# Kernel tuning notes

Measured on AMD Instinct MI355X. Metric: run time of the kernel, lower is better.

The kernel has to match this reference:

```python
import jax, jax.numpy as jnp
import numpy as np

B, D, WIN, SW = 256, 38, 640, 10
S = WIN // SW  # 64 time steps
EPS = 1e-5

def leaky(v):
    return jnp.where(v > 0, v, 0.01 * v)

def _ln(v, g, b):
    mu = v.mean(-1, keepdims=True)
    var = v.var(-1, keepdims=True)
    return g * (v - mu) / jnp.sqrt(var + EPS) + b

def setup_inputs():
    key = jax.random.key(0)
    ks = jax.random.split(key, 24)
    n = lambda k, shp, s=0.05: jax.random.normal(k, shp, jnp.float32) * s
    return {
        'x': jax.random.normal(ks[0], (B, D, WIN), jnp.float32),
        'W1': n(ks[1], (D, 64, SW)), 'b1': n(ks[2], (D, 64)),
        'W2': n(ks[3], (D, 4, 3)), 'b2': n(ks[4], (D, 4)),
        'Wl': n(ks[5], (D, 64, 124)), 'bl': n(ks[6], (D, 64)),
        'Wb1': n(ks[7], (64, 64)), 'bb1': n(ks[8], (64,)),
        'lng': jnp.ones((64,), jnp.float32), 'lnb': jnp.zeros((64,), jnp.float32),
        'Wb2': n(ks[9], (64, 64)), 'bb2': n(ks[10], (64,)),
        'Wq': n(ks[11], (1, 64)), 'bq': n(ks[12], (1,)),
        'Wk': n(ks[13], (D, 64)), 'bk': n(ks[14], (D,)),
        'Wv1': n(ks[15], (D, 32, 64)), 'bv1': n(ks[16], (D, 32)),
        'lnvg': jnp.ones((D, 32), jnp.float32), 'lnvb': jnp.zeros((D, 32), jnp.float32),
        'Wv2': n(ks[17], (D, 32)), 'bv2': n(ks[18], (D,)),
        'Wq2': n(ks[19], (1, 64 * D)), 'bq2': n(ks[20], (1,)),
        'Wk2': n(ks[21], (S, 64 * D)), 'bk2': n(ks[22], (S,)),
    }

def reference(x, W1, b1, W2, b2, Wl, bl, Wb1, bb1, lng, lnb, Wb2, bb2,
              Wq, bq, Wk, bk, Wv1, bv1, lnvg, lnvb, Wv2, bv2, Wq2, bq2, Wk2, bk2):
    Bsz = x.shape[0]
    # FE1: per-channel Conv1d(1,64,k=SW,stride=SW) == window-reshape + per-dim GEMM
    xw = x.reshape(Bsz, D, S, SW)
    f1 = leaky(jnp.einsum('bdsw,dow->bdso', xw, W1) + b1[None, :, None, :])  # [B,D,S,64]
    # FE2: per-channel Conv1d(1,4,k=3,p=1) over the 64 features
    xp = jnp.pad(f1, ((0, 0), (0, 0), (0, 0), (1, 1)))
    win = jnp.stack([xp[..., r:r + 64] for r in range(3)], -1)  # [B,D,S,64,3]
    c = leaky(jnp.einsum('bdstr,dcr->bdsct', win, W2) + b2[None, :, None, :, None])  # [B,D,S,4,64]
    # MaxPool1d(3, stride=2): 64 -> 31
    m = jnp.max(jnp.stack([c[..., s:s + 61:2] for s in range(3)], 0), 0)  # [B,D,S,4,31]
    e = leaky(jnp.einsum('bdsf,dof->bdso', m.reshape(Bsz, D, S, 124), Wl) + bl[None, :, None, :])  # embed [B,D,S,64]
    # BeforeInstanceEncoder (shared), recurrent accumulator == cumsum over time
    h = leaky(_ln(jnp.einsum('bdso,po->bdsp', e, Wb1) + bb1, lng, lnb))
    g = leaky(jnp.einsum('bdsp,qp->bdsq', h, Wb2) + bb2)
    acml = jnp.cumsum(g, axis=2)  # [B,D,S,64]
    wq = jax.nn.sigmoid(jnp.einsum('bdso,o->bds', e, Wq[0]) + bq[0])            # [B,D,S]
    wk = jax.nn.sigmoid(jnp.einsum('bdso,jo->bdsj', acml, Wk) + bk)             # [B,D,S,D]
    att1 = jax.nn.softmax(jnp.einsum('bks,bjsk->bsj', wq, wk) / np.float32(np.sqrt(D)), axis=-1)  # [B,S,D]
    v = leaky(_ln(jnp.einsum('bdso,dho->bdsh', e, Wv1) + bv1[None, :, None, :],
                  lnvg[None, :, None, :], lnvb[None, :, None, :]))
    wv = jax.nn.relu(jnp.einsum('bdsh,dh->bds', v, Wv2) + bv2[None, :, None])   # [B,D,S]
    cont1 = jnp.transpose(wv, (0, 2, 1)) * att1  # [B,S,D]
    contributes1 = cont1[..., None]              # [B,S,D,1]
    output1 = cont1.sum(-1, keepdims=True)       # [B,S,1]
    # bag-level attention over time
    ef = jnp.transpose(e, (0, 2, 1, 3)).reshape(Bsz, S, D * 64)
    wq_a = jax.nn.sigmoid(ef @ Wq2.T + bq2)[..., 0]  # [B,S]
    wk_a = jax.nn.sigmoid(ef @ Wk2.T + bk2)          # [B,S,S]
    att2 = jax.nn.softmax(jnp.einsum('bs,bts->bt', wq_a, wk_a) / np.float32(np.sqrt(WIN)), axis=-1)  # [B,S]
    contributes2 = output1 * att2[..., None]  # [B,S,1]
    output2 = contributes2.sum(1)             # [B,1]
    return (output2, contributes2, contributes1)
```

## Files before the change

### kernel.cpp

```cpp
#include <hip/hip_runtime.h>
#include <math.h>

#define Bv 256
#define Dv 38
#define Sv 64
#define SWv 10
#define EPSv 1e-5f

typedef float f4 __attribute__((ext_vector_type(4)));

__device__ __forceinline__ float leaky(float v){ return v > 0.f ? v : 0.01f*v; }
__device__ __forceinline__ float sigm(float v){ return 1.f/(1.f+expf(-v)); }

__device__ __forceinline__ float wred64(float v){
  #pragma unroll
  for (int off=32; off; off>>=1) v += __shfl_xor(v, off, 64);
  return v;
}
__device__ __forceinline__ float wmax64(float v){
  #pragma unroll
  for (int off=32; off; off>>=1) v = fmaxf(v, __shfl_xor(v, off, 64));
  return v;
}

__global__ __launch_bounds__(256) void k0_pack(
    const float* __restrict__ Wl, const float* __restrict__ W1,
    const float* __restrict__ Wv1,
    float* __restrict__ wlT, float* __restrict__ w1T, float* __restrict__ wv1T)
{
  int idx = blockIdx.x*256 + threadIdx.x;
  if (idx < 330752) {
    int d = idx / 8704, r = idx % 8704;
    int c = r / 1088, rr = r % 1088;
    int q = rr / 68, o = rr % 68;
    int ch = q >> 2, io = q & 3, fi = 4*c + io;
    float v = 0.f;
    if (o < 64 && fi <= 30) v = Wl[d*7936 + o*124 + ch*31 + fi];
    wlT[idx] = v;
  } else if (idx < 330752 + 25840) {
    int t = idx - 330752;
    int d = t / 680, rr = t % 680;
    int w = rr / 68, o = rr % 68;
    w1T[t] = (o < 64) ? W1[d*640 + o*10 + w] : 0.f;
  } else if (idx < 330752 + 25840 + 87552) {
    int t = idx - 330752 - 25840;
    int d = t / 2304, rr = t % 2304;
    int o = rr / 36, h = rr % 36;
    wv1T[t] = (h < 32) ? Wv1[d*2048 + h*64 + o] : 0.f;
  }
}

__global__ __launch_bounds__(256, 3) void k1_fe4(
    const float* __restrict__ x,
    const float* __restrict__ w1T_all, const float* __restrict__ b1,
    const float* __restrict__ W2, const float* __restrict__ b2,
    const float* __restrict__ wlT_all, const float* __restrict__ bl,
    const float* __restrict__ Wq, const float* __restrict__ bq,
    const float* __restrict__ wv1T_all, const float* __restrict__ bv1,
    const float* __restrict__ lnvg, const float* __restrict__ lnvb,
    const float* __restrict__ Wv2, const float* __restrict__ bv2,
    const float* __restrict__ Wq2,
    float* __restrict__ e_ws, float* __restrict__ wq2_ws, float* __restrict__ wv_ws,
    float* __restrict__ wqa_p)
{
  __shared__ float sm[12688];
  const int d  = blockIdx.x >> 7;
  const int b0 = (blockIdx.x & 127) * 2;
  const int tid = threadIdx.x;
  const int z = tid >> 7;
  const int t = tid & 127;
  const int tx = t & 15, ty = t >> 4;
  const int wz = ty >> 2;
  const int bd = (b0 + z)*Dv + d;
  const float bq0 = bq[0];

#define PJ(j) ((j) < 4 ? 4*ty + (j) : 32 + 4*ty + ((j)-4))

  if (tid < 64) {
    sm[12032+tid] = b1[d*64+tid];
    sm[12096+tid] = bl[d*64+tid];
    sm[12160+tid] = Wq[tid];
    sm[12368+tid] = Wq2[d*64+tid];
  } else if (tid < 96) {
    int u = tid-64;
    sm[12240+u]=bv1[d*32+u]; sm[12272+u]=lnvg[d*32+u];
    sm[12304+u]=lnvb[d*32+u]; sm[12336+u]=Wv2[d*32+u];
  } else if (tid < 108) sm[12224+(tid-96)] = W2[d*12+(tid-96)];
  else if (tid < 112)   sm[12236+(tid-108)] = b2[d*4+(tid-108)];

  {
    const f4* s4 = (const f4*)(w1T_all + (size_t)d*680);
    if (tid < 170) ((f4*)&sm[9792])[tid] = s4[tid];
  }
  for (int i = tid; i < 1280; i += 256) {
    int z2 = i / 640, tt = i % 640;
    sm[10472 + z2*680 + (tt%10)*68 + tt/10] =
      x[((size_t)((b0+z2)*Dv + d))*640 + tt];
  }
  const f4* wlsrc = (const f4*)(wlT_all + (size_t)d*8704);
  {
    ((f4*)&sm[8704])[tid] = wlsrc[tid];
    if (tid < 16) ((f4*)&sm[8704])[tid+256] = wlsrc[tid+256];
  }
  __syncthreads();

  float fe[4][8];
  #pragma unroll
  for (int i=0;i<4;++i)
    #pragma unroll
    for (int j=0;j<8;++j) fe[i][j]=0.f;
  #pragma unroll
  for (int w = 0; w < 10; ++w) {
    f4 a   = *(const f4*)&sm[10472 + z*680 + w*68 + 4*tx];
    f4 blo = *(const f4*)&sm[9792 + w*68 + 4*ty];
    f4 bhi = *(const f4*)&sm[9792 + w*68 + 32 + 4*ty];
    #pragma unroll
    for (int i=0;i<4;++i)
      #pragma unroll
      for (int j=0;j<8;++j) fe[i][j] += a[i]*((j<4)?blo[j&3]:bhi[j&3]);
  }
  #pragma unroll
  for (int j=0;j<8;++j) {
    int o = PJ(j);
    float bb = sm[12032+o];
    f4 v = {leaky(fe[0][j]+bb), leaky(fe[1][j]+bb), leaky(fe[2][j]+bb), leaky(fe[3][j]+bb)};
    *(f4*)&sm[z*4352 + o*68 + 4*tx] = v;
  }
  __syncthreads();

  float ea[4][8];
  #pragma unroll
  for (int i=0;i<4;++i)
    #pragma unroll
    for (int j=0;j<8;++j) ea[i][j]=0.f;

  f4 wr0, wr1;
  for (int c = 0; c < 8; ++c) {
    if (c > 0) {
      ((f4*)&sm[8704])[tid] = wr0;
      if (tid < 16) ((f4*)&sm[8704])[tid+256] = wr1;
    }
    {
      int sg = t & 15, io = (t >> 4) & 3, chh = t >> 6;
      int fi = 4*c + io;
      if (fi <= 30) {
        int t0 = 2*fi - 1;
        const float* fsrc = &sm[z*4352];
        f4 v0;
        if (fi == 0) { v0[0]=0.f; v0[1]=0.f; v0[2]=0.f; v0[3]=0.f; }
        else         { v0 = *(const f4*)&fsrc[t0*68 + 4*sg]; }
        f4 v1 = *(const f4*)&fsrc[(t0+1)*68 + 4*sg];
        f4 v2 = *(const f4*)&fsrc[(t0+2)*68 + 4*sg];
        f4 v3 = *(const f4*)&fsrc[(t0+3)*68 + 4*sg];
        f4 v4 = *(const f4*)&fsrc[(t0+4)*68 + 4*sg];
        float* mdst = &sm[9792 + z*1088];
        #pragma unroll
        for (int cc2 = 0; cc2 < 2; ++cc2) {
          int ch = 2*chh + cc2;
          float w0=sm[12224+ch*3], w1=sm[12224+ch*3+1], w2=sm[12224+ch*3+2];
          float bb=sm[12236+ch];
          f4 r;
          #pragma unroll
          for (int e2=0;e2<4;++e2) {
            float ca = bb + v0[e2]*w0 + v1[e2]*w1 + v2[e2]*w2;
            float cb = bb + v1[e2]*w0 + v2[e2]*w1 + v3[e2]*w2;
            float cc = bb + v2[e2]*w0 + v3[e2]*w1 + v4[e2]*w2;
            r[e2] = fmaxf(fmaxf(leaky(ca),leaky(cb)),leaky(cc));
          }
          *(f4*)&mdst[(ch*4+io)*68 + 4*sg] = r;
        }
      }
    }
    if (c < 7) {
      wr0 = wlsrc[(c+1)*272 + tid];
      if (tid < 16) wr1 = wlsrc[(c+1)*272 + 256 + tid];
    }
    __syncthreads();
    {
      const float* ma = &sm[9792 + z*1088];
      #pragma unroll
      for (int q=0;q<16;++q){
        f4 a   = *(const f4*)&ma[q*68+4*tx];
        f4 blo = *(const f4*)&sm[8704 + q*68+4*ty];
        f4 bhi = *(const f4*)&sm[8704 + q*68+32+4*ty];
        #pragma unroll
        for (int i=0;i<4;++i)
          #pragma unroll
          for (int j=0;j<8;++j) ea[i][j] += a[i]*((j<4)?blo[j&3]:bhi[j&3]);
      }
    }
    __syncthreads();
  }

  float ev[4][8];
  #pragma unroll
  for (int i=0;i<4;++i)
    #pragma unroll
    for (int j=0;j<8;++j) ev[i][j] = leaky(ea[i][j] + sm[12096 + PJ(j)]);

  {
    float* erow = e_ws + (size_t)bd * 4096;
    #pragma unroll
    for (int i=0;i<4;++i) {
      f4 lo = {ev[i][0],ev[i][1],ev[i][2],ev[i][3]};
      f4 hi = {ev[i][4],ev[i][5],ev[i][6],ev[i][7]};
      *(f4*)&erow[(4*tx+i)*64 + 4*ty] = lo;
      *(f4*)&erow[(4*tx+i)*64 + 32 + 4*ty] = hi;
    }
  }
  #pragma unroll
  for (int j=0;j<8;++j) {
    int o = PJ(j);
    f4 v = {ev[0][j],ev[1][j],ev[2][j],ev[3][j]};
    *(f4*)&sm[z*4352 + o*68 + 4*tx] = v;
  }
  #pragma unroll
  for (int i=0;i<4;++i) {
    float p = 0.f, pa = 0.f;
    #pragma unroll
    for (int j=0;j<8;++j) {
      p  += ev[i][j]*sm[12160 + PJ(j)];
      pa += ev[i][j]*sm[12368 + PJ(j)];
    }
    p += __shfl_xor(p, 16);  p += __shfl_xor(p, 32);
    pa += __shfl_xor(pa, 16); pa += __shfl_xor(pa, 32);
    if ((ty & 3) == 0) {
      sm[11520 + z*128 + wz*64 + 4*tx + i] = p;
      sm[12432 + z*128 + wz*64 + 4*tx + i] = pa;
    }
  }
  {
    const f4* s4 = (const f4*)(wv1T_all + (size_t)d*2304);
    f4 a0 = s4[tid], a1 = s4[tid+256];
    ((f4*)&sm[8704])[tid] = a0;
    ((f4*)&sm[8704])[tid+256] = a1;
    if (tid < 64) ((f4*)&sm[8704])[tid+512] = s4[tid+512];
  }
  __syncthreads();

  if (tid < 128) {
    int z2 = tid >> 6, r = tid & 63;
    float p = sm[11520 + z2*128 + r] + sm[11520 + z2*128 + 64 + r];
    wq2_ws[((size_t)(b0+z2)*64 + r)*Dv + d] = sigm(p + bq0);
    float pa = sm[12432 + z2*128 + r] + sm[12432 + z2*128 + 64 + r];
    wqa_p[((size_t)(b0+z2)*64 + r)*Dv + d] = pa;
  }

  float va[4][4];
  #pragma unroll
  for (int i=0;i<4;++i)
    #pragma unroll
    for (int j=0;j<4;++j) va[i][j]=0.f;
  #pragma unroll 8
  for (int o = 0; o < 64; ++o) {
    f4 a  = *(const f4*)&sm[z*4352 + o*68 + 4*tx];
    f4 bb = *(const f4*)&sm[8704 + o*36 + 4*ty];
    #pragma unroll
    for (int i=0;i<4;++i)
      #pragma unroll
      for (int j=0;j<4;++j) va[i][j] += a[i]*bb[j];
  }
  #pragma unroll
  for (int i=0;i<4;++i)
    #pragma unroll
    for (int j=0;j<4;++j) va[i][j] += sm[12240 + 4*ty + j];

  #pragma unroll
  for (int i=0;i<4;++i) {
    float ps=0.f, pq=0.f;
    #pragma unroll
    for (int j=0;j<4;++j) { ps += va[i][j]; pq += va[i][j]*va[i][j]; }
    ps += __shfl_xor(ps, 16); ps += __shfl_xor(ps, 32);
    pq += __shfl_xor(pq, 16); pq += __shfl_xor(pq, 32);
    if ((ty & 3) == 0) {
      sm[11008 + z*128 + wz*64 + 4*tx + i] = ps;
      sm[11264 + z*128 + wz*64 + 4*tx + i] = pq;
    }
  }
  __syncthreads();
  if (tid < 128) {
    int z2 = tid >> 6, r = tid & 63;
    float s_ = sm[11008 + z2*128 + r] + sm[11008 + z2*128 + 64 + r];
    float q_ = sm[11264 + z2*128 + r] + sm[11264 + z2*128 + 64 + r];
    float mu = s_*(1.f/32.f);
    float vr = q_*(1.f/32.f) - mu*mu;
    sm[11776 + z2*64 + r] = mu;
    sm[11904 + z2*64 + r] = rsqrtf(vr + EPSv);
  }
  __syncthreads();

  #pragma unroll
  for (int i=0;i<4;++i) {
    float mu = sm[11776 + z*64 + 4*tx + i];
    float rs = sm[11904 + z*64 + 4*tx + i];
    float p = 0.f;
    #pragma unroll
    for (int j=0;j<4;++j) {
      int h = 4*ty + j;
      float vh = leaky(sm[12272+h]*(va[i][j]-mu)*rs + sm[12304+h]);
      p += vh*sm[12336+h];
    }
    p += __shfl_xor(p, 16);
    p += __shfl_xor(p, 32);
    if ((ty & 3) == 0) sm[11520 + z*128 + wz*64 + 4*tx + i] = p;
  }
  __syncthreads();
  if (tid < 128) {
    int z2 = tid >> 6, r = tid & 63;
    float p = sm[11520 + z2*128 + r] + sm[11520 + z2*128 + 64 + r];
    wv_ws[((size_t)((b0+z2)*Dv + d))*64 + r] = fmaxf(p + bv2[d], 0.f);
  }
#undef PJ
}

__global__ __launch_bounds__(256) void k2_fused(
    const float* __restrict__ e_ws,
    const float* __restrict__ Wb1, const float* __restrict__ bb1,
    const float* __restrict__ lng, const float* __restrict__ lnb,
    const float* __restrict__ Wb2, const float* __restrict__ bb2,
    const float* __restrict__ Wk, const float* __restrict__ bk,
    const float* __restrict__ wq2_ws, float* __restrict__ score1)
{
  __shared__ float smem[14080];
  float* bufA = smem;
  float* bufB = smem + 8448;
  float* pts  = smem + 12544;
  float* ptq  = smem + 13184;
  float* stmu = smem + 13824;
  float* strs = smem + 13952;

  const int tid = threadIdx.x;
  const int tx = tid & 31;
  const int ty = tid >> 5;
  const int wid = tid >> 6;
  const int lane = tid & 63;
  const int bd0 = blockIdx.x * 2;
  const int bd1 = bd0 + 1;

#define PJ(j) ((j) < 4 ? 4*ty + (j) : 32 + 4*ty + ((j)-4))

  const int r0 = tid & 15, c0 = tid >> 4;

  f4 w2r[4];
  {
    const f4* W2src = (const f4*)Wb2;
    #pragma unroll
    for (int q = 0; q < 4; ++q) w2r[q] = W2src[(r0+16*q)*16 + c0];
  }

  {
    const f4* Esrc  = (const f4*)(e_ws + (size_t)bd0 * 4096);
    #pragma unroll
    for (int q = 0; q < 8; ++q) {
      int r = r0 + 16*q;
      f4 v = Esrc[r*16 + c0];
      #pragma unroll
      for (int k = 0; k < 4; ++k) bufA[(4*c0+k)*132 + r] = v[k];
    }
    const f4* W1src = (const f4*)Wb1;
    #pragma unroll
    for (int q = 0; q < 4; ++q) {
      int rr = r0 + 16*q;
      f4 v1 = W1src[rr*16 + c0];
      #pragma unroll
      for (int k = 0; k < 4; ++k) bufB[(4*c0+k)*64 + rr] = v1[k];
    }
  }
  __syncthreads();

  float bb1v[8], lngv[8], lnbv[8], bb2v[8];
  #pragma unroll
  for (int j=0;j<8;++j) {
    int p = PJ(j);
    bb1v[j]=bb1[p]; lngv[j]=lng[p]; lnbv[j]=lnb[p]; bb2v[j]=bb2[p];
  }

  float h[4][8];
  #pragma unroll
  for (int i=0;i<4;++i)
    #pragma unroll
    for (int j=0;j<8;++j) h[i][j]=0.f;
  for (int o = 0; o < 64; ++o) {
    f4 a  = *(const f4*)(bufA + o*132 + 4*tx);
    f4 bl = *(const f4*)(bufB + o*64 + 4*ty);
    f4 bh = *(const f4*)(bufB + o*64 + 32 + 4*ty);
    #pragma unroll
    for (int i=0;i<4;++i)
      #pragma unroll
      for (int j=0;j<8;++j) h[i][j] += a[i]*((j<4)?bl[j&3]:bh[j&3]);
  }
  #pragma unroll
  for (int i=0;i<4;++i)
    #pragma unroll
    for (int j=0;j<8;++j) h[i][j] += bb1v[j];

  #pragma unroll
  for (int i=0;i<4;++i) {
    float ps=0.f, pq=0.f;
    #pragma unroll
    for (int j=0;j<8;++j) { ps += h[i][j]; pq += h[i][j]*h[i][j]; }
    ps += __shfl_xor(ps, 32);
    pq += __shfl_xor(pq, 32);
    if (lane < 32) { pts[(4*tx+i)*5 + wid] = ps; ptq[(4*tx+i)*5 + wid] = pq; }
  }
  __syncthreads();

  {
    #pragma unroll
    for (int q = 0; q < 4; ++q) {
      int rr = r0 + 16*q;
      f4 v = w2r[q];
      #pragma unroll
      for (int k = 0; k < 4; ++k) bufB[(4*c0+k)*64 + rr] = v[k];
    }
  }
  float wkr[10];
  #pragma unroll
  for (int n = 0; n < 10; ++n) {
    int i2 = tid + 256*n;
    int q = i2/40, k = i2%40;
    wkr[n] = (k < Dv) ? Wk[k*64 + q] : 0.f;
  }
  if (tid < 128) {
    float s = pts[tid*5]+pts[tid*5+1]+pts[tid*5+2]+pts[tid*5+3];
    float q = ptq[tid*5]+ptq[tid*5+1]+ptq[tid*5+2]+ptq[tid*5+3];
    float mu = s*(1.f/64.f);
    float va = q*(1.f/64.f) - mu*mu;
    stmu[tid] = mu;
    strs[tid] = rsqrtf(va + EPSv);
  }
  __syncthreads();

  {
    float muv[4], rsv[4];
    #pragma unroll
    for (int i=0;i<4;++i) { muv[i]=stmu[4*tx+i]; rsv[i]=strs[4*tx+i]; }
    #pragma unroll
    for (int j=0;j<8;++j) {
      f4 v;
      #pragma unroll
      for (int i=0;i<4;++i)
        v[i] = leaky(lngv[j]*(h[i][j]-muv[i])*rsv[i] + lnbv[j]);
      *(f4*)&bufA[PJ(j)*132 + 4*tx] = v;
    }
  }
  __syncthreads();

  float g[4][8];
  #pragma unroll
  for (int i=0;i<4;++i)
    #pragma unroll
    for (int j=0;j<8;++j) g[i][j]=0.f;
  for (int p = 0; p < 64; ++p) {
    f4 a  = *(const f4*)(bufA + p*132 + 4*tx);
    f4 bl = *(const f4*)(bufB + p*64 + 4*ty);
    f4 bh = *(const f4*)(bufB + p*64 + 32 + 4*ty);
    #pragma unroll
    for (int i=0;i<4;++i)
      #pragma unroll
      for (int j=0;j<8;++j) g[i][j] += a[i]*((j<4)?bl[j&3]:bh[j&3]);
  }
  #pragma unroll
  for (int i=0;i<4;++i)
    #pragma unroll
    for (int j=0;j<8;++j) g[i][j] = leaky(g[i][j] + bb2v[j]);

  #pragma unroll
  for (int j=0;j<8;++j) {
    float c0_=g[0][j], c1=c0_+g[1][j], c2=c1+g[2][j], c3=c2+g[3][j];
    float incl = c3;
    #pragma unroll
    for (int dd=1; dd<16; dd<<=1) {
      float t = __shfl_up(incl, dd, 16);
      if ((tid & 15) >= dd) incl += t;
    }
    float ex = incl - c3;
    g[0][j]=ex+c0_; g[1][j]=ex+c1; g[2][j]=ex+c2; g[3][j]=ex+c3;
  }
  __syncthreads();

  #pragma unroll
  for (int j=0;j<8;++j) {
    f4 v = {g[0][j], g[1][j], g[2][j], g[3][j]};
    *(f4*)&bufA[PJ(j)*132 + 4*tx] = v;
  }
  #pragma unroll
  for (int n = 0; n < 10; ++n) bufB[tid + 256*n] = wkr[n];
  __syncthreads();

  float u[4][4], u2[4][4];
  #pragma unroll
  for (int i=0;i<4;++i)
    #pragma unroll
    for (int j=0;j<4;++j) { u[i][j]=0.f; u2[i][j]=0.f; }
  for (int q = 0; q < 64; ++q) {
    f4 a   = *(const f4*)(bufA + q*132 + 4*tx);
    f4 b1v = *(const f4*)(bufB + q*40 + 4*ty);
    #pragma unroll
    for (int i=0;i<4;++i)
      #pragma unroll
      for (int j=0;j<4;++j) u[i][j] += a[i]*b1v[j];
    if (ty < 2) {
      f4 b2v = *(const f4*)(bufB + q*40 + 32 + 4*ty);
      #pragma unroll
      for (int i=0;i<4;++i)
        #pragma unroll
        for (int j=0;j<4;++j) u2[i][j] += a[i]*b2v[j];
    }
  }

  const int b0g = bd0/Dv, d0g = bd0%Dv, b1g = bd1/Dv, d1g = bd1%Dv;
  #pragma unroll
  for (int i=0;i<4;++i) {
    int r = 4*tx + i;
    int s = r & 63;
    int bb_ = (r >> 6) ? b1g : b0g;
    const float* wqrow = wq2_ws + ((size_t)bb_*Sv + s)*Dv;
    float p = 0.f;
    #pragma unroll
    for (int j=0;j<4;++j) {
      int k = 4*ty + j;
      p += sigm(u[i][j] + bk[k]) * wqrow[k];
    }
    if (ty < 2) {
      #pragma unroll
      for (int j=0;j<4;++j) {
        int k = 32 + 4*ty + j;
        if (k < Dv) p += sigm(u2[i][j] + bk[k]) * wqrow[k];
      }
    }
    p += __shfl_xor(p, 32);
    if (lane < 32) pts[r*5 + wid] = p;
  }
  __syncthreads();
  if (tid < 128) {
    float tot = pts[tid*5]+pts[tid*5+1]+pts[tid*5+2]+pts[tid*5+3];
    int grp = tid >> 6, s = tid & 63;
    int bb_ = grp ? b1g : b0g;
    int dd_ = grp ? d1g : d0g;
    score1[((size_t)bb_*Sv + s)*Dv + dd_] = tot;
  }
#undef PJ
}

__global__ __launch_bounds__(64) void k3_att1(
    const float* __restrict__ score1, const float* __restrict__ wv_ws,
    const float* __restrict__ wqa_p, const float* __restrict__ bq2,
    float* __restrict__ out_c1, float* __restrict__ output1, float* __restrict__ wq_a)
{
  const int blk = blockIdx.x;
  const int b = blk / Sv, s = blk % Sv;
  const int lane = threadIdx.x;

  const float invsq = 0.16222142113076254f;
  float sc = (lane<Dv) ? score1[(b*Sv+s)*Dv+lane]*invsq : -1e30f;
  float mx = wmax64(sc);
  float ex = (lane<Dv) ? expf(sc-mx) : 0.f;
  float den = wred64(ex);
  float att = ex/den;
  float c1 = 0.f;
  if (lane<Dv) {
    c1 = wv_ws[(b*Dv+lane)*Sv+s]*att;
    out_c1[(b*Sv+s)*Dv+lane] = c1;
  }
  float tot = wred64(c1);
  if (lane==0) output1[b*Sv+s] = tot;

  float p = (lane < Dv) ? wqa_p[((size_t)b*Sv + s)*Dv + lane] : 0.f;
  p = wred64(p);
  if (lane==0) wq_a[b*Sv+s] = sigm(p + bq2[0]);
}

__global__ __launch_bounds__(256) void k4_gemm(
    const float* __restrict__ e_ws, const float* __restrict__ Wk2, const float* __restrict__ bk2,
    const float* __restrict__ wq_a, float* __restrict__ score2)
{
  const int b = blockIdx.x;
  const int tid = threadIdx.x;
  const int tx = tid & 15, ty = tid >> 4;
  __shared__ float AsT[64*68];
  __shared__ float BsT[64*68];
  __shared__ float pt[64*17];

  float acc[4][4];
  #pragma unroll
  for (int i=0;i<4;++i)
    #pragma unroll
    for (int j=0;j<4;++j) acc[i][j]=0.f;

  const int r0 = tid & 15, oc0 = tid >> 4;
  const f4* Bsrc = (const f4*)Wk2;

  for (int d = 0; d < 38; ++d) {
    const f4* Asrc = (const f4*)(e_ws + ((size_t)(b*Dv+d))*4096);
    #pragma unroll
    for (int q = 0; q < 4; ++q) {
      int r = r0 + 16*q;
      f4 av = Asrc[r*16 + oc0];
      f4 bv = Bsrc[(size_t)r*608 + d*16 + oc0];
      #pragma unroll
      for (int k = 0; k < 4; ++k) {
        AsT[(4*oc0+k)*68 + r] = av[k];
        BsT[(4*oc0+k)*68 + r] = bv[k];
      }
    }
    __syncthreads();
    #pragma unroll 4
    for (int o = 0; o < 64; ++o) {
      f4 a  = *(const f4*)&AsT[o*68 + 4*tx];
      f4 bb = *(const f4*)&BsT[o*68 + 4*ty];
      #pragma unroll
      for (int i=0;i<4;++i)
        #pragma unroll
        for (int j=0;j<4;++j) acc[i][j] += a[i]*bb[j];
    }
    __syncthreads();
  }

  #pragma unroll
  for (int i=0;i<4;++i) {
    float p = 0.f;
    #pragma unroll
    for (int j=0;j<4;++j) {
      int s = 4*ty + j;
      p += sigm(acc[i][j] + bk2[s]) * wq_a[b*Sv + s];
    }
    pt[(4*tx+i)*17 + ty] = p;
  }
  __syncthreads();
  if (tid < 64) {
    float tot = 0.f;
    #pragma unroll
    for (int y=0;y<16;++y) tot += pt[tid*17+y];
    score2[b*Sv + tid] = tot;
  }
}

__global__ __launch_bounds__(64) void k5_final(
    const float* __restrict__ score2, const float* __restrict__ output1,
    float* __restrict__ out)
{
  const int b = blockIdx.x;
  const int lane = threadIdx.x;
  const float inv = 0.039528470752104741f;
  float v = score2[b*Sv+lane]*inv;
  float mx = wmax64(v);
  float ex = expf(v-mx);
  float den = wred64(ex);
  float att = ex/den;
  float c2 = output1[b*Sv+lane]*att;
  out[256 + b*Sv + lane] = c2;
  float tot = wred64(c2);
  if (lane==0) out[b] = tot;
}

extern "C" void kernel_launch(void* const* d_in, const int* in_sizes, int n_in,
                              void* d_out, int out_size, void* d_ws, size_t ws_size,
                              hipStream_t stream)
{
  const float* x    = (const float*)d_in[0];
  const float* W1   = (const float*)d_in[1];
  const float* b1   = (const float*)d_in[2];
  const float* W2   = (const float*)d_in[3];
  const float* b2   = (const float*)d_in[4];
  const float* Wl   = (const float*)d_in[5];
  const float* bl   = (const float*)d_in[6];
  const float* Wb1  = (const float*)d_in[7];
  const float* bb1  = (const float*)d_in[8];
  const float* lng  = (const float*)d_in[9];
  const float* lnb  = (const float*)d_in[10];
  const float* Wb2  = (const float*)d_in[11];
  const float* bb2  = (const float*)d_in[12];
  const float* Wq   = (const float*)d_in[13];
  const float* bq   = (const float*)d_in[14];
  const float* Wk   = (const float*)d_in[15];
  const float* bk   = (const float*)d_in[16];
  const float* Wv1  = (const float*)d_in[17];
  const float* bv1  = (const float*)d_in[18];
  const float* lnvg = (const float*)d_in[19];
  const float* lnvb = (const float*)d_in[20];
  const float* Wv2  = (const float*)d_in[21];
  const float* bv2  = (const float*)d_in[22];
  const float* Wq2  = (const float*)d_in[23];
  const float* bq2  = (const float*)d_in[24];
  const float* Wk2  = (const float*)d_in[25];
  const float* bk2  = (const float*)d_in[26];

  float* ws = (float*)d_ws;
  float* e_ws  = ws;
  float* wq2w  = e_ws + (size_t)Bv*Dv*Sv*64;
  float* wv_ws = wq2w + (size_t)Bv*Sv*Dv;
  float* sc1   = wv_ws + (size_t)Bv*Dv*Sv;
  float* out1  = sc1 + (size_t)Bv*Sv*Dv;
  float* wqa   = out1 + (size_t)Bv*Sv;
  float* sc2   = wqa + (size_t)Bv*Sv;
  float* wlT   = sc2 + (size_t)Bv*Sv;
  float* w1T   = wlT + 330752;
  float* wv1T  = w1T + 25840;
  float* wqap  = wv1T + 87552;

  float* out = (float*)d_out;
  float* out_c1 = out + 256 + Bv*Sv;

  hipLaunchKernelGGL(k0_pack, dim3(1736), dim3(256), 0, stream,
    Wl, W1, Wv1, wlT, w1T, wv1T);
  hipLaunchKernelGGL(k1_fe4, dim3(Dv*128), dim3(256), 0, stream,
    x, w1T, b1, W2, b2, wlT, bl, Wq, bq, wv1T, bv1, lnvg, lnvb, Wv2, bv2,
    Wq2, e_ws, wq2w, wv_ws, wqap);
  hipLaunchKernelGGL(k2_fused, dim3(Bv*Dv/2), dim3(256), 0, stream,
    e_ws, Wb1, bb1, lng, lnb, Wb2, bb2, Wk, bk, wq2w, sc1);
  hipLaunchKernelGGL(k3_att1, dim3(Bv*Sv), dim3(64), 0, stream,
    sc1, wv_ws, wqap, bq2, out_c1, out1, wqa);
  hipLaunchKernelGGL(k4_gemm, dim3(Bv), dim3(256), 0, stream,
    e_ws, Wk2, bk2, wqa, sc2);
  hipLaunchKernelGGL(k5_final, dim3(Bv), dim3(64), 0, stream, sc2, out1, out);
}
```

Baseline: 663.5 us.

## Store embeddings transposed and pre-pack weights to remove in-kernel transposes

The embedding workspace is now written feature-major by the feature-extraction kernel, and Wb1, Wb2, Wk and Wk2 are pre-transposed in the packing kernel. Downstream kernels can then stage tiles into shared memory with contiguous vector stores instead of scalar transposing scatters. LayerNorm partial sums are now accumulated with shared-memory atomics rather than per-wave slots plus a reduction pass, which removes one barrier. The cost is a larger packing kernel, about 150K extra packed floats in the workspace, and shared atomics in k2.

```diff
diff --git a/kernel.cpp b/kernel.cpp
--- a/kernel.cpp
+++ b/kernel.cpp
@@ -25,8 +25,12 @@
 
 __global__ __launch_bounds__(256) void k0_pack(
     const float* __restrict__ Wl, const float* __restrict__ W1,
-    const float* __restrict__ Wv1,
-    float* __restrict__ wlT, float* __restrict__ w1T, float* __restrict__ wv1T)
+    const float* __restrict__ Wv1, const float* __restrict__ Wb1,
+    const float* __restrict__ Wb2, const float* __restrict__ Wk,
+    const float* __restrict__ Wk2,
+    float* __restrict__ wlT, float* __restrict__ w1T, float* __restrict__ wv1T,
+    float* __restrict__ wb1T, float* __restrict__ wb2T, float* __restrict__ wkT,
+    float* __restrict__ wk2T)
 {
   int idx = blockIdx.x*256 + threadIdx.x;
   if (idx < 330752) {
@@ -37,16 +41,33 @@
     float v = 0.f;
     if (o < 64 && fi <= 30) v = Wl[d*7936 + o*124 + ch*31 + fi];
     wlT[idx] = v;
-  } else if (idx < 330752 + 25840) {
+  } else if (idx < 356592) {
     int t = idx - 330752;
     int d = t / 680, rr = t % 680;
     int w = rr / 68, o = rr % 68;
     w1T[t] = (o < 64) ? W1[d*640 + o*10 + w] : 0.f;
-  } else if (idx < 330752 + 25840 + 87552) {
-    int t = idx - 330752 - 25840;
+  } else if (idx < 444144) {
+    int t = idx - 356592;
     int d = t / 2304, rr = t % 2304;
     int o = rr / 36, h = rr % 36;
     wv1T[t] = (h < 32) ? Wv1[d*2048 + h*64 + o] : 0.f;
+  } else if (idx < 448240) {
+    int t = idx - 444144;
+    int o = t >> 6, p = t & 63;
+    wb1T[t] = Wb1[p*64 + o];
+  } else if (idx < 452336) {
+    int t = idx - 448240;
+    int p = t >> 6, q = t & 63;
+    wb2T[t] = Wb2[q*64 + p];
+  } else if (idx < 454896) {
+    int t = idx - 452336;
+    int q = t / 40, k = t % 40;
+    wkT[t] = (k < Dv) ? Wk[k*64 + q] : 0.f;
+  } else if (idx < 610544) {
+    int t = idx - 454896;
+    int d = t / 4096, rr = t % 4096;
+    int o = rr >> 6, s = rr & 63;
+    wk2T[t] = Wk2[s*2432 + d*64 + o];
   }
 }
 
@@ -60,7 +81,7 @@
     const float* __restrict__ lnvg, const float* __restrict__ lnvb,
     const float* __restrict__ Wv2, const float* __restrict__ bv2,
     const float* __restrict__ Wq2,
-    float* __restrict__ e_ws, float* __restrict__ wq2_ws, float* __restrict__ wv_ws,
+    float* __restrict__ e_wsT, float* __restrict__ wq2_ws, float* __restrict__ wv_ws,
     float* __restrict__ wqa_p)
 {
   __shared__ float sm[12688];
@@ -199,13 +220,11 @@
     for (int j=0;j<8;++j) ev[i][j] = leaky(ea[i][j] + sm[12096 + PJ(j)]);
 
   {
-    float* erow = e_ws + (size_t)bd * 4096;
-    #pragma unroll
-    for (int i=0;i<4;++i) {
-      f4 lo = {ev[i][0],ev[i][1],ev[i][2],ev[i][3]};
-      f4 hi = {ev[i][4],ev[i][5],ev[i][6],ev[i][7]};
-      *(f4*)&erow[(4*tx+i)*64 + 4*ty] = lo;
-      *(f4*)&erow[(4*tx+i)*64 + 32 + 4*ty] = hi;
+    float* erow = e_wsT + (size_t)bd * 4096;
+    #pragma unroll
+    for (int j=0;j<8;++j) {
+      f4 v = {ev[0][j],ev[1][j],ev[2][j],ev[3][j]};
+      *(f4*)&erow[PJ(j)*64 + 4*tx] = v;
     }
   }
   #pragma unroll
@@ -314,56 +333,51 @@
 }
 
 __global__ __launch_bounds__(256) void k2_fused(
-    const float* __restrict__ e_ws,
-    const float* __restrict__ Wb1, const float* __restrict__ bb1,
+    const float* __restrict__ e_wsT,
+    const float* __restrict__ wb1T, const float* __restrict__ bb1,
     const float* __restrict__ lng, const float* __restrict__ lnb,
-    const float* __restrict__ Wb2, const float* __restrict__ bb2,
-    const float* __restrict__ Wk, const float* __restrict__ bk,
+    const float* __restrict__ wb2T, const float* __restrict__ bb2,
+    const float* __restrict__ wkT, const float* __restrict__ bk,
     const float* __restrict__ wq2_ws, float* __restrict__ score1)
 {
-  __shared__ float smem[14080];
+  __shared__ float smem[12864];
   float* bufA = smem;
   float* bufB = smem + 8448;
   float* pts  = smem + 12544;
-  float* ptq  = smem + 13184;
-  float* stmu = smem + 13824;
-  float* strs = smem + 13952;
+  float* ptq  = smem + 12704;
 
   const int tid = threadIdx.x;
   const int tx = tid & 31;
   const int ty = tid >> 5;
-  const int wid = tid >> 6;
   const int lane = tid & 63;
   const int bd0 = blockIdx.x * 2;
   const int bd1 = bd0 + 1;
 
 #define PJ(j) ((j) < 4 ? 4*ty + (j) : 32 + 4*ty + ((j)-4))
 
-  const int r0 = tid & 15, c0 = tid >> 4;
+  if (tid < 128) { pts[tid] = 0.f; ptq[tid] = 0.f; }
 
   f4 w2r[4];
   {
-    const f4* W2src = (const f4*)Wb2;
-    #pragma unroll
-    for (int q = 0; q < 4; ++q) w2r[q] = W2src[(r0+16*q)*16 + c0];
+    const f4* s4 = (const f4*)wb2T;
+    #pragma unroll
+    for (int q = 0; q < 4; ++q) w2r[q] = s4[tid + 256*q];
   }
 
   {
-    const f4* Esrc  = (const f4*)(e_ws + (size_t)bd0 * 4096);
-    #pragma unroll
-    for (int q = 0; q < 8; ++q) {
-      int r = r0 + 16*q;
-      f4 v = Esrc[r*16 + c0];
-      #pragma unroll
-      for (int k = 0; k < 4; ++k) bufA[(4*c0+k)*132 + r] = v[k];
-    }
-    const f4* W1src = (const f4*)Wb1;
-    #pragma unroll
-    for (int q = 0; q < 4; ++q) {
-      int rr = r0 + 16*q;
-      f4 v1 = W1src[rr*16 + c0];
-      #pragma unroll
-      for (int k = 0; k < 4; ++k) bufB[(4*c0+k)*64 + rr] = v1[k];
+    const f4* Esrc = (const f4*)(e_wsT + (size_t)bd0 * 4096);
+    #pragma unroll
+    for (int m = 0; m < 8; ++m) {
+      int n = tid + 256*m;
+      int o = n >> 5, t5 = n & 31;
+      int z = t5 >> 4, sg = t5 & 15;
+      *(f4*)&bufA[o*132 + z*64 + 4*sg] = Esrc[z*1024 + o*16 + sg];
+    }
+    const f4* W1s = (const f4*)wb1T;
+    #pragma unroll
+    for (int m = 0; m < 4; ++m) {
+      int n = tid + 256*m;
+      ((f4*)bufB)[n] = W1s[n];
     }
   }
   __syncthreads();
@@ -401,40 +415,26 @@
     for (int j=0;j<8;++j) { ps += h[i][j]; pq += h[i][j]*h[i][j]; }
     ps += __shfl_xor(ps, 32);
     pq += __shfl_xor(pq, 32);
-    if (lane < 32) { pts[(4*tx+i)*5 + wid] = ps; ptq[(4*tx+i)*5 + wid] = pq; }
+    if (lane < 32) {
+      atomicAdd(&pts[4*tx+i], ps);
+      atomicAdd(&ptq[4*tx+i], pq);
+    }
   }
   __syncthreads();
 
   {
     #pragma unroll
-    for (int q = 0; q < 4; ++q) {
-      int rr = r0 + 16*q;
-      f4 v = w2r[q];
-      #pragma unroll
-      for (int k = 0; k < 4; ++k) bufB[(4*c0+k)*64 + rr] = v[k];
-    }
-  }
-  float wkr[10];
-  #pragma unroll
-  for (int n = 0; n < 10; ++n) {
-    int i2 = tid + 256*n;
-    int q = i2/40, k = i2%40;
-    wkr[n] = (k < Dv) ? Wk[k*64 + q] : 0.f;
-  }
-  if (tid < 128) {
-    float s = pts[tid*5]+pts[tid*5+1]+pts[tid*5+2]+pts[tid*5+3];
-    float q = ptq[tid*5]+ptq[tid*5+1]+ptq[tid*5+2]+ptq[tid*5+3];
-    float mu = s*(1.f/64.f);
-    float va = q*(1.f/64.f) - mu*mu;
-    stmu[tid] = mu;
-    strs[tid] = rsqrtf(va + EPSv);
-  }
-  __syncthreads();
-
+    for (int q = 0; q < 4; ++q) ((f4*)bufB)[tid + 256*q] = w2r[q];
+  }
   {
     float muv[4], rsv[4];
     #pragma unroll
-    for (int i=0;i<4;++i) { muv[i]=stmu[4*tx+i]; rsv[i]=strs[4*tx+i]; }
+    for (int i=0;i<4;++i) {
+      float s = pts[4*tx+i], q = ptq[4*tx+i];
+      float mu = s*(1.f/64.f);
+      float va = q*(1.f/64.f) - mu*mu;
+      muv[i] = mu; rsv[i] = rsqrtf(va + EPSv);
+    }
     #pragma unroll
     for (int j=0;j<8;++j) {
       f4 v;
@@ -445,6 +445,8 @@
     }
   }
   __syncthreads();
+
+  if (tid < 128) pts[tid] = 0.f;
 
   float g[4][8];
   #pragma unroll
@@ -477,6 +479,10 @@
     float ex = incl - c3;
     g[0][j]=ex+c0_; g[1][j]=ex+c1; g[2][j]=ex+c2; g[3][j]=ex+c3;
   }
+
+  float wkr[10];
+  #pragma unroll
+  for (int n = 0; n < 10; ++n) wkr[n] = wkT[tid + 256*n];
   __syncthreads();
 
   #pragma unroll
@@ -530,11 +536,11 @@
       }
     }
     p += __shfl_xor(p, 32);
-    if (lane < 32) pts[r*5 + wid] = p;
+    if (lane < 32) atomicAdd(&pts[r], p);
   }
   __syncthreads();
   if (tid < 128) {
-    float tot = pts[tid*5]+pts[tid*5+1]+pts[tid*5+2]+pts[tid*5+3];
+    float tot = pts[tid];
     int grp = tid >> 6, s = tid & 63;
     int bb_ = grp ? b1g : b0g;
     int dd_ = grp ? d1g : d0g;
@@ -572,7 +578,8 @@
 }
 
 __global__ __launch_bounds__(256) void k4_gemm(
-    const float* __restrict__ e_ws, const float* __restrict__ Wk2, const float* __restrict__ bk2,
+    const float* __restrict__ e_wsT, const float* __restrict__ wk2T,
+    const float* __restrict__ bk2,
     const float* __restrict__ wq_a, float* __restrict__ score2)
 {
   const int b = blockIdx.x;
@@ -588,21 +595,15 @@
     #pragma unroll
     for (int j=0;j<4;++j) acc[i][j]=0.f;
 
-  const int r0 = tid & 15, oc0 = tid >> 4;
-  const f4* Bsrc = (const f4*)Wk2;
-
   for (int d = 0; d < 38; ++d) {
-    const f4* Asrc = (const f4*)(e_ws + ((size_t)(b*Dv+d))*4096);
-    #pragma unroll
-    for (int q = 0; q < 4; ++q) {
-      int r = r0 + 16*q;
-      f4 av = Asrc[r*16 + oc0];
-      f4 bv = Bsrc[(size_t)r*608 + d*16 + oc0];
-      #pragma unroll
-      for (int k = 0; k < 4; ++k) {
-        AsT[(4*oc0+k)*68 + r] = av[k];
-        BsT[(4*oc0+k)*68 + r] = bv[k];
-      }
+    const f4* Asrc = (const f4*)(e_wsT + ((size_t)(b*Dv+d))*4096);
+    const f4* Bsrc = (const f4*)(wk2T + (size_t)d*4096);
+    #pragma unroll
+    for (int m = 0; m < 4; ++m) {
+      int n = tid + 256*m;
+      int o = n >> 4, sg = n & 15;
+      *(f4*)&AsT[o*68 + 4*sg] = Asrc[n];
+      *(f4*)&BsT[o*68 + 4*sg] = Bsrc[n];
     }
     __syncthreads();
     #pragma unroll 4
@@ -687,8 +688,8 @@
   const float* bk2  = (const float*)d_in[26];
 
   float* ws = (float*)d_ws;
-  float* e_ws  = ws;
-  float* wq2w  = e_ws + (size_t)Bv*Dv*Sv*64;
+  float* e_wsT = ws;
+  float* wq2w  = e_wsT + (size_t)Bv*Dv*Sv*64;
   float* wv_ws = wq2w + (size_t)Bv*Sv*Dv;
   float* sc1   = wv_ws + (size_t)Bv*Dv*Sv;
   float* out1  = sc1 + (size_t)Bv*Sv*Dv;
@@ -698,20 +699,24 @@
   float* w1T   = wlT + 330752;
   float* wv1T  = w1T + 25840;
   float* wqap  = wv1T + 87552;
+  float* wb1T  = wqap + (size_t)Bv*Sv*Dv;
+  float* wb2T  = wb1T + 4096;
+  float* wkT   = wb2T + 4096;
+  float* wk2T  = wkT + 2560;
 
   float* out = (float*)d_out;
   float* out_c1 = out + 256 + Bv*Sv;
 
-  hipLaunchKernelGGL(k0_pack, dim3(1736), dim3(256), 0, stream,
-    Wl, W1, Wv1, wlT, w1T, wv1T);
+  hipLaunchKernelGGL(k0_pack, dim3(2385), dim3(256), 0, stream,
+    Wl, W1, Wv1, Wb1, Wb2, Wk, Wk2, wlT, w1T, wv1T, wb1T, wb2T, wkT, wk2T);
   hipLaunchKernelGGL(k1_fe4, dim3(Dv*128), dim3(256), 0, stream,
     x, w1T, b1, W2, b2, wlT, bl, Wq, bq, wv1T, bv1, lnvg, lnvb, Wv2, bv2,
-    Wq2, e_ws, wq2w, wv_ws, wqap);
+    Wq2, e_wsT, wq2w, wv_ws, wqap);
   hipLaunchKernelGGL(k2_fused, dim3(Bv*Dv/2), dim3(256), 0, stream,
-    e_ws, Wb1, bb1, lng, lnb, Wb2, bb2, Wk, bk, wq2w, sc1);
+    e_wsT, wb1T, bb1, lng, lnb, wb2T, bb2, wkT, bk, wq2w, sc1);
   hipLaunchKernelGGL(k3_att1, dim3(Bv*Sv), dim3(64), 0, stream,
     sc1, wv_ws, wqap, bq2, out_c1, out1, wqa);
   hipLaunchKernelGGL(k4_gemm, dim3(Bv), dim3(256), 0, stream,
-    e_ws, Wk2, bk2, wqa, sc2);
+    e_wsT, wk2T, bk2, wqa, sc2);
   hipLaunchKernelGGL(k5_final, dim3(Bv), dim3(64), 0, stream, sc2, out1, out);
 }
```

Measured after the change: 602.8 us (median of 2 runs). -9.2%, faster.
